# Kernel tuning notes

Hardware: AMD Instinct MI355X
Metric: run time of the kernel (lower is better)

## Reference

```python
import jax, jax.numpy as jnp
import numpy as np

MAX_N_LATENT = 8
EOS_THRESHOLD = 0.7
EOS_PATTERN_LEN = 3
COS_SIM_THRESHOLD = 0.3
EOS_SOFT_THRESHOLD = 0.5
CONTEXT_WINDOW = 2
EPS = 1e-8


def setup_inputs() -> dict:
    key = jax.random.key(0)
    k = jax.random.split(key, 8)
    B, S, D = 8, 4096, 1024
    s = 0.02
    latent_states = jax.random.normal(k[0], (B, S, D), dtype=jnp.float32)
    binary_mask = jax.random.randint(k[1], (B, S, 1), 0, 2).astype(jnp.int32)
    proj_w = jax.random.normal(k[2], (D, D), dtype=jnp.float32) * s
    proj_b = jax.random.normal(k[3], (D,), dtype=jnp.float32) * s
    eos_w1 = jax.random.normal(k[4], (D, D // 2), dtype=jnp.float32) * s
    eos_b1 = jax.random.normal(k[5], (D // 2,), dtype=jnp.float32) * s
    eos_w2 = jax.random.normal(k[6], (D // 2, 1), dtype=jnp.float32) * s
    eos_b2 = jax.random.normal(k[7], (1,), dtype=jnp.float32) * s
    return {"latent_states": latent_states, "binary_mask": binary_mask,
            "proj_w": proj_w, "proj_b": proj_b,
            "eos_w1": eos_w1, "eos_b1": eos_b1,
            "eos_w2": eos_w2, "eos_b2": eos_b2}


def reference(latent_states, binary_mask, proj_w, proj_b, eos_w1, eos_b1, eos_w2, eos_b2):
    B, S, D = latent_states.shape

    # ---- EOS scores (computed under no_grad in the original) ----
    h = jax.nn.relu(jnp.einsum('bsd,df->bsf', latent_states, eos_w1) + eos_b1)
    eos_scores = jax.nn.sigmoid(jnp.einsum('bsf,fo->bso', h, eos_w2) + eos_b2)[..., 0]
    eos_scores = jax.lax.stop_gradient(eos_scores)  # [B, S]

    # ---- segment ids: a boundary (mask==1) at i closes the patch that includes i ----
    m = binary_mask[..., 0].astype(jnp.int32)                 # [B, S]
    seg = jnp.cumsum(m, axis=1) - m                           # exclusive cumsum => patch id per token
    valid = (seg < MAX_N_LATENT).astype(latent_states.dtype)  # drop patches beyond MAX_N_LATENT (p[:max_patches])
    onehot = jax.nn.one_hot(jnp.clip(seg, 0, MAX_N_LATENT - 1), MAX_N_LATENT,
                            dtype=latent_states.dtype) * valid[..., None]  # [B, S, P]
    sums = jnp.einsum('bsp,bsd->bpd', onehot, latent_states)  # segmented sum
    counts = onehot.sum(axis=1)                               # [B, P]
    pooled = sums / jnp.maximum(counts, 1.0)[..., None]       # mean pooling; empty patches -> 0 (proj adds bias, as in torch)
    patches = jnp.einsum('bpd,do->bpo', pooled, proj_w) + proj_b  # [B, MAX_N_LATENT, output_dim]

    # ---- EOS bounds ----
    mthr = eos_scores > EOS_THRESHOLD
    run = mthr
    for t in range(1, EOS_PATTERN_LEN):                       # consecutive_eos_count >= EOS_PATTERN_LEN
        run = run & jnp.pad(mthr[:, :-t], ((0, 0), (t, 0)))
    a = latent_states[:, 1:-1]                                # prev state at i-1, for i >= 2
    b = latent_states[:, 2:]                                  # current state at i
    cos = (a * b).sum(-1) / (jnp.maximum(jnp.linalg.norm(a, axis=-1), EPS)
                             * jnp.maximum(jnp.linalg.norm(b, axis=-1), EPS))
    cos_rule = jnp.pad((cos < COS_SIM_THRESHOLD) & (eos_scores[:, 2:] > EOS_SOFT_THRESHOLD),
                       ((0, 0), (2, 0)))
    eos_any = run | cos_rule                                  # [B, S] (duplicate triggers don't change min/max)
    has = eos_any.any()
    idx = jnp.arange(S)[None, :]
    first = jnp.min(jnp.where(eos_any, idx, S))
    last = jnp.max(jnp.where(eos_any, idx, -1))
    start = jnp.maximum(0, first - CONTEXT_WINDOW)
    end = jnp.minimum(S - 1, last + CONTEXT_WINDOW)
    eos_bounds = jnp.where(has, jnp.stack([start, end]), jnp.full((2,), -1))
    return patches, eos_bounds
```

## Files before the change

kernel.cpp:

```cpp
#include <hip/hip_runtime.h>
#include <hip/hip_fp16.h>
#include <cstdint>
#include <cstddef>

#define B_ 8
#define S_ 4096
#define D_ 1024
#define H_ 512
#define M_ (B_*S_)

typedef __attribute__((ext_vector_type(8))) _Float16 half8;
typedef __attribute__((ext_vector_type(16))) float f16v;

union HU { int4 v; half8 h; };

__device__ inline unsigned short f2h(float f){
  _Float16 h = (_Float16)f;
  return __builtin_bit_cast(unsigned short, h);
}

__global__ __launch_bounds__(256) void k_pre(const float* __restrict__ X,
    float* __restrict__ n2o, float* __restrict__ dto, unsigned short* __restrict__ Xh,
    const float* __restrict__ w1, unsigned short* __restrict__ w1t,
    const int* __restrict__ mask, int* __restrict__ cb, float* __restrict__ logit,
    float* __restrict__ gsums, float* __restrict__ gcnt, int* __restrict__ fl){
  __shared__ float tile[32][33];
  __shared__ int sc[256];
  int bid = blockIdx.x, tid = threadIdx.x;
  if (bid < 512){
    int wave = tid>>6, lane = tid&63;
    int g0 = (bid*4 + wave)*16;
    const float4* Xv = (const float4*)X;
    ushort4* Xhv = (ushort4*)Xh;
    float4 pv[4];
    if ((g0 & (S_-1)) != 0){
      size_t bb = (size_t)(g0-1)*256;
      #pragma unroll
      for (int q=0;q<4;q++) pv[q] = Xv[bb + q*64 + lane];
    } else {
      #pragma unroll
      for (int q=0;q<4;q++) pv[q] = make_float4(0.f,0.f,0.f,0.f);
    }
    for (int r=0;r<16;r++){
      int g = g0 + r;
      size_t bb = (size_t)g*256;
      float4 cv[4];
      #pragma unroll
      for (int q=0;q<4;q++) cv[q] = Xv[bb + q*64 + lane];
      float n2=0.f, dp=0.f;
      #pragma unroll
      for (int q=0;q<4;q++){
        n2 += cv[q].x*cv[q].x + cv[q].y*cv[q].y + cv[q].z*cv[q].z + cv[q].w*cv[q].w;
        dp += pv[q].x*cv[q].x + pv[q].y*cv[q].y + pv[q].z*cv[q].z + pv[q].w*cv[q].w;
      }
      #pragma unroll
      for (int q=0;q<4;q++){
        ushort4 u;
        u.x = f2h(cv[q].x); u.y = f2h(cv[q].y); u.z = f2h(cv[q].z); u.w = f2h(cv[q].w);
        Xhv[bb + q*64 + lane] = u;
      }
      #pragma unroll
      for (int off=32; off>0; off>>=1){
        n2 += __shfl_down(n2, off);
        dp += __shfl_down(dp, off);
      }
      if (lane==0){
        n2o[g] = n2;
        if ((g & (S_-1)) != 0) dto[g-1] = dp;
      }
      #pragma unroll
      for (int q=0;q<4;q++) pv[q] = cv[q];
    }
  } else if (bid < 1024){
    int b = bid - 512;
    int n0 = (b&15)*32, k0 = (b>>4)*32;
    int tx = tid&31, ty = tid>>5;
    #pragma unroll
    for (int i=0;i<4;i++) tile[ty+8*i][tx] = w1[(size_t)(k0+ty+8*i)*H_ + n0+tx];
    __syncthreads();
    #pragma unroll
    for (int i=0;i<4;i++) w1t[(size_t)(n0+ty+8*i)*D_ + k0+tx] = f2h(tile[tx][ty+8*i]);
  } else {
    int bb = bid - 1024;
    const int* mrow = mask + (size_t)bb*S_ + tid*16;
    int s = 0;
    #pragma unroll
    for (int i=0;i<16;i++) s += mrow[i];
    sc[tid] = s;
    __syncthreads();
    for (int off=1; off<256; off<<=1){
      int v = (tid>=off) ? sc[tid-off] : 0;
      __syncthreads();
      sc[tid] += v;
      __syncthreads();
    }
    if ((tid & 15) == 0) cb[bb*16 + (tid>>4)] = (tid==0) ? 0 : sc[tid-1];
    float4* lz = (float4*)(logit + bb*4096);
    #pragma unroll
    for (int e=tid; e<1024; e+=256) lz[e] = make_float4(0.f,0.f,0.f,0.f);
    float4* gz = (float4*)(gsums + (size_t)bb*8192);
    for (int e=tid; e<2048; e+=256) gz[e] = make_float4(0.f,0.f,0.f,0.f);
    if (bb==0){
      if (tid < 64) gcnt[tid] = 0.f;
      if (tid == 64){ fl[0] = 0x7FFFFFFF; fl[1] = -1; fl[2] = 0; }
    }
  }
}

#define AS1 __attribute__((address_space(1)))
#define AS3 __attribute__((address_space(3)))

#define STAGE(kt_, nb_) do { int k0e = (kt_)*32; \
  char* abase = (char*)As[nb_]; char* bbase = (char*)Bs[nb_]; \
  _Pragma("unroll") for (int q=0;q<2;q++){ \
    __builtin_amdgcn_global_load_lds((const AS1 void*)(agp[q]+k0e), (AS3 void*)(abase+aldo[q]),16,0,0); \
    __builtin_amdgcn_global_load_lds((const AS1 void*)(bgp[q]+k0e), (AS3 void*)(bbase+bldo[q]),16,0,0); } \
} while(0)

__global__ __launch_bounds__(256) void k_mlp(const unsigned short* __restrict__ Xh,
    const unsigned short* __restrict__ W1T, const float* __restrict__ b1,
    const float* __restrict__ w2, float* __restrict__ logit){
  __shared__ __align__(16) unsigned short As[2][128*32];
  __shared__ __align__(16) unsigned short Bs[2][128*32];
  int tid = threadIdx.x;
  int wave = tid>>6, lane = tid&63;
  int l31 = lane&31, h = lane>>5;
  int m0 = (blockIdx.x & 255)*128, n0 = (blockIdx.x >> 8)*128;
  int wm = (wave>>1)*64, wn = (wave&1)*64;
  f16v acc[2][2] = {};

  int srow = lane>>2;
  const unsigned short* agp[2]; const unsigned short* bgp[2];
  unsigned aldo[2], bldo[2];
  #pragma unroll
  for (int q=0;q<2;q++){
    int rb = wave*32 + q*16;
    int r  = rb + srow;
    int c  = (lane&3) ^ ((r>>1)&3);
    agp[q] = Xh  + (size_t)(m0 + r)*D_ + c*8;
    bgp[q] = W1T + (size_t)(n0 + r)*D_ + c*8;
    aldo[q] = rb*64;
    bldo[q] = rb*64;
  }

  unsigned aoff[2][2], boff[2][2];
  #pragma unroll
  for (int i=0;i<2;i++){
    int rm = wm + 32*i + l31;
    int rn = wn + 32*i + l31;
    #pragma unroll
    for (int kk=0;kk<2;kk++){
      int c = kk*2 + h;
      aoff[i][kk] = rm*64 + ((c ^ ((rm>>1)&3))<<4);
      boff[i][kk] = rn*64 + ((c ^ ((rn>>1)&3))<<4);
    }
  }

  float b1v[2], w2v[2];
  #pragma unroll
  for (int j=0;j<2;j++){
    int n = n0 + wn + 32*j + l31;
    b1v[j] = b1[n]; w2v[j] = w2[n];
  }

  STAGE(0, 0);
  for (int kt=0; kt<32; ++kt){
    __syncthreads();
    if (kt < 31) STAGE(kt+1, (kt+1)&1);
    const char* ab = (const char*)As[kt&1];
    const char* bb = (const char*)Bs[kt&1];
    #pragma unroll
    for (int kk=0;kk<2;kk++){
      HU a0, a1, b0, b1u;
      a0.v  = *(const int4*)(ab + aoff[0][kk]);
      a1.v  = *(const int4*)(ab + aoff[1][kk]);
      b0.v  = *(const int4*)(bb + boff[0][kk]);
      b1u.v = *(const int4*)(bb + boff[1][kk]);
      acc[0][0] = __builtin_amdgcn_mfma_f32_32x32x16_f16(a0.h, b0.h,  acc[0][0], 0,0,0);
      acc[0][1] = __builtin_amdgcn_mfma_f32_32x32x16_f16(a0.h, b1u.h, acc[0][1], 0,0,0);
      acc[1][0] = __builtin_amdgcn_mfma_f32_32x32x16_f16(a1.h, b0.h,  acc[1][0], 0,0,0);
      acc[1][1] = __builtin_amdgcn_mfma_f32_32x32x16_f16(a1.h, b1u.h, acc[1][1], 0,0,0);
    }
  }

  #pragma unroll
  for (int i=0;i<2;i++){
    #pragma unroll
    for (int r=0;r<16;r++){
      float p = w2v[0]*fmaxf(acc[i][0][r] + b1v[0], 0.f)
              + w2v[1]*fmaxf(acc[i][1][r] + b1v[1], 0.f);
      p += __shfl_xor(p, 1);
      p += __shfl_xor(p, 2);
      p += __shfl_xor(p, 4);
      p += __shfl_xor(p, 8);
      p += __shfl_xor(p, 16);
      if (l31 == 0){
        int row = m0 + wm + 32*i + (r&3) + 8*(r>>2) + 4*h;
        atomicAdd(&logit[row], p);
      }
    }
  }
}

__global__ void k_pool(const float* __restrict__ X, const int* __restrict__ mask,
                       const int* __restrict__ cb, float* __restrict__ gsums,
                       float* __restrict__ gcnt){
  int c = blockIdx.x, b = blockIdx.y, tid = threadIdx.x;
  int base = cb[b*16 + c];
  if (base >= 8) return;
  __shared__ float lsum[8*1024];
  __shared__ int seg[256];
  __shared__ float lcnt[8];
  __shared__ int send_s;
  for (int e=tid; e<8192; e+=256) lsum[e] = 0.f;
  if (tid==0){
    float cnts[8] = {0,0,0,0,0,0,0,0};
    const int* mrow = mask + (size_t)b*S_ + c*256;
    int running = base, i = 0;
    for (; i<256; ++i){
      if (running >= 8) break;
      seg[i] = running;
      cnts[running] += 1.f;
      running += mrow[i];
    }
    send_s = i;
    #pragma unroll
    for (int p=0;p<8;p++) lcnt[p] = cnts[p];
  }
  __syncthreads();
  int send = send_s;
  for (int s2=0; s2<send; ++s2){
    int sg = seg[s2];
    size_t gb = ((size_t)(b*S_ + c*256 + s2))*D_;
    #pragma unroll
    for (int q=0;q<4;q++){
      int d = tid + q*256;
      lsum[sg*1024 + d] += X[gb + d];
    }
  }
  __syncthreads();
  for (int e=tid; e<8192; e+=256){
    float v = lsum[e];
    if (v != 0.f) atomicAdd(&gsums[(size_t)b*8192 + e], v);
  }
  if (tid < 8){
    float v = lcnt[tid];
    if (v != 0.f) atomicAdd(&gcnt[b*8 + tid], v);
  }
}

__global__ __launch_bounds__(256) void k_patch(const float* __restrict__ gsums,
                        const float* __restrict__ gcnt,
                        const float* __restrict__ pw, const float* __restrict__ pb,
                        float* __restrict__ out){
  __shared__ float pool[8192];
  __shared__ float red[2048];
  int b = blockIdx.y, cx = blockIdx.x, tid = threadIdx.x;
  const float4* gs4 = (const float4*)(gsums + (size_t)b*8192);
  float4* pool4 = (float4*)pool;
  for (int e4=tid; e4<2048; e4+=256){
    int p = e4>>8;
    float inv = 1.f / fmaxf(gcnt[b*8 + p], 1.f);
    float4 v = gs4[e4];
    v.x*=inv; v.y*=inv; v.z*=inv; v.w*=inv;
    pool4[e4] = v;
  }
  __syncthreads();
  int c = tid & 31, ks = tid >> 5;
  int col = cx*32 + c;
  float acc[8] = {0,0,0,0,0,0,0,0};
  for (int k=ks*128; k<ks*128+128; ++k){
    float w = pw[(size_t)k*D_ + col];
    #pragma unroll
    for (int p=0;p<8;p++) acc[p] += pool[p*1024 + k]*w;
  }
  #pragma unroll
  for (int p=0;p<8;p++) red[tid*8 + p] = acc[p];
  __syncthreads();
  {
    int p = tid>>5, cc = tid&31;
    float s = 0.f;
    #pragma unroll
    for (int k2=0;k2<8;k2++) s += red[(k2*32 + cc)*8 + p];
    out[(size_t)(b*8+p)*D_ + cx*32 + cc] = s + pb[cx*32 + cc];
  }
}

__global__ void k_flagsb(const float* __restrict__ logit, const float* __restrict__ n2,
                        const float* __restrict__ dt, const float* __restrict__ b2p,
                        int* __restrict__ fl, float* __restrict__ ob){
  int g = blockIdx.x*256 + threadIdx.x;
  float b2 = b2p[0];
  int s = g & (S_-1);
  bool any = false;
  if (s >= 2){
    float z0 = logit[g] + b2;
    float z1 = logit[g-1] + b2;
    float z2 = logit[g-2] + b2;
    const float THR = 0.8472978603872037f;
    bool run = (z0 > THR) & (z1 > THR) & (z2 > THR);
    float na = fmaxf(sqrtf(n2[g-1]), 1e-8f);
    float nb = fmaxf(sqrtf(n2[g]), 1e-8f);
    bool cosr = (dt[g-1] < 0.3f*na*nb) & (z0 > 0.f);
    any = run | cosr;
  }
  int mn = any ? s : 0x7FFFFFFF;
  int mx = any ? s : -1;
  #pragma unroll
  for (int off=32; off>0; off>>=1){
    mn = min(mn, __shfl_down(mn, off));
    mx = max(mx, __shfl_down(mx, off));
  }
  if ((threadIdx.x & 63) == 0){
    atomicMin(&fl[0], mn);
    atomicMax(&fl[1], mx);
  }
  __syncthreads();
  if (threadIdx.x == 0){
    __threadfence();
    int old = atomicAdd(&fl[2], 1);
    if (old == gridDim.x - 1){
      int f = atomicMin(&fl[0], 0x7FFFFFFF);
      int l = atomicMax(&fl[1], (int)0x80000000);
      if (l < 0){ ob[0] = -1.f; ob[1] = -1.f; }
      else {
        int st = f - 2; if (st < 0) st = 0;
        int en = l + 2; if (en > S_-1) en = S_-1;
        ob[0] = (float)st; ob[1] = (float)en;
      }
    }
  }
}

extern "C" void kernel_launch(void* const* d_in, const int* in_sizes, int n_in,
                              void* d_out, int out_size, void* d_ws, size_t ws_size,
                              hipStream_t stream){
  const float* latent = (const float*)d_in[0];
  const int*   mask   = (const int*)d_in[1];
  const float* proj_w = (const float*)d_in[2];
  const float* proj_b = (const float*)d_in[3];
  const float* eos_w1 = (const float*)d_in[4];
  const float* eos_b1 = (const float*)d_in[5];
  const float* eos_w2 = (const float*)d_in[6];
  const float* eos_b2 = (const float*)d_in[7];
  float* out = (float*)d_out;

  char* ws = (char*)d_ws;
  unsigned short* W1T = (unsigned short*)ws;
  unsigned short* Xh  = (unsigned short*)(ws + 1048576);
  float* fbase = (float*)(ws + 1048576 + 67108864);
  float* logit = fbase;
  float* norm2 = fbase + 32768;
  float* dotv  = fbase + 65536;
  float* gsums = fbase + 98304;
  float* gcnt  = fbase + 163840;
  int* chunkbase = (int*)(fbase + 163904);
  int* fl        = (int*)(fbase + 164032);

  k_pre<<<1032, 256, 0, stream>>>(latent, norm2, dotv, Xh, eos_w1, W1T, mask,
                                  chunkbase, logit, gsums, gcnt, fl);
  k_pool<<<dim3(16,8), 256, 0, stream>>>(latent, mask, chunkbase, gsums, gcnt);
  k_patch<<<dim3(32,8), 256, 0, stream>>>(gsums, gcnt, proj_w, proj_b, out);
  k_mlp<<<1024, 256, 0, stream>>>(Xh, W1T, eos_b1, eos_w2, logit);
  k_flagsb<<<128, 256, 0, stream>>>(logit, norm2, dotv, eos_b2, fl, out + 65536);
}
```

Baseline: 307.5 us.

## Switch EOS MLP GEMM from fp16 to fp8 with scaled weights

Converts the latent activations and transposed eos_w1 to fp8 instead of fp16, with the weights prescaled by 64 and the scale undone through b1 and w2 in the epilogue. The GEMM now uses fp8 MFMA with 64-byte K tiles and a new LDS swizzle, plus a per-block rotation of the K start to spread memory traffic. This halves the bytes written in k_pre and read in k_mlp and raises matrix throughput. In exchange it loses precision in the eos scores, which can flip threshold comparisons near 0.5 or 0.7.

```diff
diff --git a/kernel.cpp b/kernel.cpp
--- a/kernel.cpp
+++ b/kernel.cpp
@@ -9,19 +9,16 @@
 #define H_ 512
 #define M_ (B_*S_)
 
-typedef __attribute__((ext_vector_type(8))) _Float16 half8;
 typedef __attribute__((ext_vector_type(16))) float f16v;
 
-union HU { int4 v; half8 h; };
-
-__device__ inline unsigned short f2h(float f){
-  _Float16 h = (_Float16)f;
-  return __builtin_bit_cast(unsigned short, h);
+__device__ inline unsigned char f2fp8(float f){
+  int v = __builtin_amdgcn_cvt_pk_fp8_f32(f, f, 0, false);
+  return (unsigned char)(v & 0xFF);
 }
 
 __global__ __launch_bounds__(256) void k_pre(const float* __restrict__ X,
-    float* __restrict__ n2o, float* __restrict__ dto, unsigned short* __restrict__ Xh,
-    const float* __restrict__ w1, unsigned short* __restrict__ w1t,
+    float* __restrict__ n2o, float* __restrict__ dto, unsigned char* __restrict__ X8,
+    const float* __restrict__ w1, unsigned char* __restrict__ w1t8,
     const int* __restrict__ mask, int* __restrict__ cb, float* __restrict__ logit,
     float* __restrict__ gsums, float* __restrict__ gcnt, int* __restrict__ fl){
   __shared__ float tile[32][33];
@@ -31,7 +28,7 @@
     int wave = tid>>6, lane = tid&63;
     int g0 = (bid*4 + wave)*16;
     const float4* Xv = (const float4*)X;
-    ushort4* Xhv = (ushort4*)Xh;
+    int* X8i = (int*)X8;
     float4 pv[4];
     if ((g0 & (S_-1)) != 0){
       size_t bb = (size_t)(g0-1)*256;
@@ -55,9 +52,9 @@
       }
       #pragma unroll
       for (int q=0;q<4;q++){
-        ushort4 u;
-        u.x = f2h(cv[q].x); u.y = f2h(cv[q].y); u.z = f2h(cv[q].z); u.w = f2h(cv[q].w);
-        Xhv[bb + q*64 + lane] = u;
+        int pk = __builtin_amdgcn_cvt_pk_fp8_f32(cv[q].x, cv[q].y, 0, false);
+        pk = __builtin_amdgcn_cvt_pk_fp8_f32(cv[q].z, cv[q].w, pk, true);
+        X8i[bb + q*64 + lane] = pk;
       }
       #pragma unroll
       for (int off=32; off>0; off>>=1){
@@ -79,7 +76,8 @@
     for (int i=0;i<4;i++) tile[ty+8*i][tx] = w1[(size_t)(k0+ty+8*i)*H_ + n0+tx];
     __syncthreads();
     #pragma unroll
-    for (int i=0;i<4;i++) w1t[(size_t)(n0+ty+8*i)*D_ + k0+tx] = f2h(tile[tx][ty+8*i]);
+    for (int i=0;i<4;i++)
+      w1t8[(size_t)(n0+ty+8*i)*D_ + k0+tx] = f2fp8(64.f * tile[tx][ty+8*i]);
   } else {
     int bb = bid - 1024;
     const int* mrow = mask + (size_t)bb*S_ + tid*16;
@@ -110,49 +108,52 @@
 #define AS1 __attribute__((address_space(1)))
 #define AS3 __attribute__((address_space(3)))
 
-#define STAGE(kt_, nb_) do { int k0e = (kt_)*32; \
+#define STAGE(ktp_, nb_) do { int k0e = (ktp_)*64; \
   char* abase = (char*)As[nb_]; char* bbase = (char*)Bs[nb_]; \
   _Pragma("unroll") for (int q=0;q<2;q++){ \
     __builtin_amdgcn_global_load_lds((const AS1 void*)(agp[q]+k0e), (AS3 void*)(abase+aldo[q]),16,0,0); \
     __builtin_amdgcn_global_load_lds((const AS1 void*)(bgp[q]+k0e), (AS3 void*)(bbase+bldo[q]),16,0,0); } \
 } while(0)
 
-__global__ __launch_bounds__(256) void k_mlp(const unsigned short* __restrict__ Xh,
-    const unsigned short* __restrict__ W1T, const float* __restrict__ b1,
+__global__ __launch_bounds__(256) void k_mlp(const unsigned char* __restrict__ X8,
+    const unsigned char* __restrict__ W1T8, const float* __restrict__ b1,
     const float* __restrict__ w2, float* __restrict__ logit){
-  __shared__ __align__(16) unsigned short As[2][128*32];
-  __shared__ __align__(16) unsigned short Bs[2][128*32];
+  __shared__ __align__(16) unsigned char As[2][128*64];
+  __shared__ __align__(16) unsigned char Bs[2][128*64];
   int tid = threadIdx.x;
   int wave = tid>>6, lane = tid&63;
   int l31 = lane&31, h = lane>>5;
   int m0 = (blockIdx.x & 255)*128, n0 = (blockIdx.x >> 8)*128;
+  int rot = (((blockIdx.x >> 8)*4) + (blockIdx.x & 3)) & 15;
   int wm = (wave>>1)*64, wn = (wave&1)*64;
   f16v acc[2][2] = {};
 
-  int srow = lane>>2;
-  const unsigned short* agp[2]; const unsigned short* bgp[2];
+  int srow = lane>>2, sslot = lane&3;
+  const unsigned char* agp[2]; const unsigned char* bgp[2];
   unsigned aldo[2], bldo[2];
   #pragma unroll
   for (int q=0;q<2;q++){
     int rb = wave*32 + q*16;
     int r  = rb + srow;
-    int c  = (lane&3) ^ ((r>>1)&3);
-    agp[q] = Xh  + (size_t)(m0 + r)*D_ + c*8;
-    bgp[q] = W1T + (size_t)(n0 + r)*D_ + c*8;
+    int y  = ((r>>1)&3) ^ ((r>>3)&3);
+    int c  = sslot ^ y;
+    agp[q] = X8  + (size_t)(m0 + r)*D_ + c*16;
+    bgp[q] = W1T8 + (size_t)(n0 + r)*D_ + c*16;
     aldo[q] = rb*64;
     bldo[q] = rb*64;
   }
 
-  unsigned aoff[2][2], boff[2][2];
+  unsigned aoff[2][4], boff[2][4];
   #pragma unroll
   for (int i=0;i<2;i++){
     int rm = wm + 32*i + l31;
     int rn = wn + 32*i + l31;
-    #pragma unroll
-    for (int kk=0;kk<2;kk++){
-      int c = kk*2 + h;
-      aoff[i][kk] = rm*64 + ((c ^ ((rm>>1)&3))<<4);
-      boff[i][kk] = rn*64 + ((c ^ ((rn>>1)&3))<<4);
+    int ym = ((rm>>1)&3) ^ ((rm>>3)&3);
+    int yn = ((rn>>1)&3) ^ ((rn>>3)&3);
+    #pragma unroll
+    for (int t=0;t<4;t++){
+      aoff[i][t] = rm*64 + ((t ^ ym)<<4) + h*8;
+      boff[i][t] = rn*64 + ((t ^ yn)<<4) + h*8;
     }
   }
 
@@ -160,26 +161,26 @@
   #pragma unroll
   for (int j=0;j<2;j++){
     int n = n0 + wn + 32*j + l31;
-    b1v[j] = b1[n]; w2v[j] = w2[n];
-  }
-
-  STAGE(0, 0);
-  for (int kt=0; kt<32; ++kt){
+    b1v[j] = b1[n] * 64.f;
+    w2v[j] = w2[n] * (1.f/64.f);
+  }
+
+  STAGE(rot, 0);
+  for (int kt=0; kt<16; ++kt){
     __syncthreads();
-    if (kt < 31) STAGE(kt+1, (kt+1)&1);
+    if (kt < 15) STAGE((kt+1+rot)&15, (kt+1)&1);
     const char* ab = (const char*)As[kt&1];
     const char* bb = (const char*)Bs[kt&1];
     #pragma unroll
-    for (int kk=0;kk<2;kk++){
-      HU a0, a1, b0, b1u;
-      a0.v  = *(const int4*)(ab + aoff[0][kk]);
-      a1.v  = *(const int4*)(ab + aoff[1][kk]);
-      b0.v  = *(const int4*)(bb + boff[0][kk]);
-      b1u.v = *(const int4*)(bb + boff[1][kk]);
-      acc[0][0] = __builtin_amdgcn_mfma_f32_32x32x16_f16(a0.h, b0.h,  acc[0][0], 0,0,0);
-      acc[0][1] = __builtin_amdgcn_mfma_f32_32x32x16_f16(a0.h, b1u.h, acc[0][1], 0,0,0);
-      acc[1][0] = __builtin_amdgcn_mfma_f32_32x32x16_f16(a1.h, b0.h,  acc[1][0], 0,0,0);
-      acc[1][1] = __builtin_amdgcn_mfma_f32_32x32x16_f16(a1.h, b1u.h, acc[1][1], 0,0,0);
+    for (int t=0;t<4;t++){
+      long a0 = *(const long*)(ab + aoff[0][t]);
+      long a1 = *(const long*)(ab + aoff[1][t]);
+      long b0 = *(const long*)(bb + boff[0][t]);
+      long b1u = *(const long*)(bb + boff[1][t]);
+      acc[0][0] = __builtin_amdgcn_mfma_f32_32x32x16_fp8_fp8(a0, b0,  acc[0][0], 0,0,0);
+      acc[0][1] = __builtin_amdgcn_mfma_f32_32x32x16_fp8_fp8(a0, b1u, acc[0][1], 0,0,0);
+      acc[1][0] = __builtin_amdgcn_mfma_f32_32x32x16_fp8_fp8(a1, b0,  acc[1][0], 0,0,0);
+      acc[1][1] = __builtin_amdgcn_mfma_f32_32x32x16_fp8_fp8(a1, b1u, acc[1][1], 0,0,0);
     }
   }
 
@@ -346,9 +347,9 @@
   float* out = (float*)d_out;
 
   char* ws = (char*)d_ws;
-  unsigned short* W1T = (unsigned short*)ws;
-  unsigned short* Xh  = (unsigned short*)(ws + 1048576);
-  float* fbase = (float*)(ws + 1048576 + 67108864);
+  unsigned char* W1T8 = (unsigned char*)ws;
+  unsigned char* X8   = (unsigned char*)(ws + 1048576);
+  float* fbase = (float*)(ws + 1048576 + 33554432);
   float* logit = fbase;
   float* norm2 = fbase + 32768;
   float* dotv  = fbase + 65536;
@@ -357,10 +358,10 @@
   int* chunkbase = (int*)(fbase + 163904);
   int* fl        = (int*)(fbase + 164032);
 
-  k_pre<<<1032, 256, 0, stream>>>(latent, norm2, dotv, Xh, eos_w1, W1T, mask,
+  k_pre<<<1032, 256, 0, stream>>>(latent, norm2, dotv, X8, eos_w1, W1T8, mask,
                                   chunkbase, logit, gsums, gcnt, fl);
   k_pool<<<dim3(16,8), 256, 0, stream>>>(latent, mask, chunkbase, gsums, gcnt);
   k_patch<<<dim3(32,8), 256, 0, stream>>>(gsums, gcnt, proj_w, proj_b, out);
-  k_mlp<<<1024, 256, 0, stream>>>(Xh, W1T, eos_b1, eos_w2, logit);
+  k_mlp<<<1024, 256, 0, stream>>>(X8, W1T8, eos_b1, eos_w2, logit);
   k_flagsb<<<128, 256, 0, stream>>>(logit, norm2, dotv, eos_b2, fl, out + 65536);
 }
```

Result: faster. 298.7 us (-2.9%).
